# Kernel optimization log

Measured on AMD Instinct MI355X. Metric: run time of the kernel, lower is better.

## Reference

```python
import jax, jax.numpy as jnp
import numpy as np

N = 100000      # nodes (spots/cells)
IN = 512        # layers[0]: gene features
HID = 128       # layers[1]: GAT out_feats (num_heads=1)
OUT = 64        # layers[-1]: embedding dim
K = 20          # clusters
E_RAND = 800000 # random edges; + N self-loops => 900000 edges total
DEC_ALPHA = 1.0
NEG_SLOPE = 0.2  # DGL GATConv default leaky_relu slope


def setup_inputs() -> dict:
    key = jax.random.key(0)
    ks = jax.random.split(key, 9)
    x = jax.random.normal(ks[0], (N, IN), dtype=jnp.float32)
    # random edges + self-loops so every node has in-degree >= 1
    src = jnp.concatenate([jax.random.randint(ks[1], (E_RAND,), 0, N), jnp.arange(N)])
    dst = jnp.concatenate([jax.random.randint(ks[2], (E_RAND,), 0, N), jnp.arange(N)])
    W_gat = jax.random.normal(ks[3], (IN, HID), dtype=jnp.float32) * (1.0 / np.sqrt(IN))
    attn_l = jax.random.normal(ks[4], (HID,), dtype=jnp.float32) * 0.1
    attn_r = jax.random.normal(ks[5], (HID,), dtype=jnp.float32) * 0.1
    bias_gat = jnp.zeros((HID,), dtype=jnp.float32)
    # nn.Linear weights stored as (in, out) so forward is x @ W (same math as x @ W_torch.T)
    W_enc = jax.random.normal(ks[6], (HID, OUT), dtype=jnp.float32) * (1.0 / np.sqrt(HID))
    W_dec = jax.random.normal(ks[7], (OUT, IN), dtype=jnp.float32) * (1.0 / np.sqrt(OUT))
    centroids = jax.random.normal(ks[8], (K, OUT), dtype=jnp.float32)
    return {"x": x, "W_gat": W_gat, "attn_l": attn_l, "attn_r": attn_r,
            "bias_gat": bias_gat, "W_enc": W_enc, "W_dec": W_dec,
            "centroids": centroids, "src": src, "dst": dst}


def reference(x, W_gat, attn_l, attn_r, bias_gat, W_enc, W_dec, centroids, src, dst):
    # --- GATConv (single head, DGL semantics) ---
    h = x @ W_gat                                  # (N, HID)
    el = h @ attn_l                                # (N,)
    er = h @ attn_r                                # (N,)
    e = jax.nn.leaky_relu(el[src] + er[dst], NEG_SLOPE)          # (E,)
    m = jax.ops.segment_max(e, dst, num_segments=N)              # per-dst max for stable softmax
    a = jnp.exp(e - m[dst])
    denom = jax.ops.segment_sum(a, dst, num_segments=N)
    alpha = a / denom[dst]                                       # edge softmax over in-edges
    agg = jax.ops.segment_sum(alpha[:, None] * h[src], dst, num_segments=N) + bias_gat  # (N, HID)
    # --- encode ---
    embed = jax.nn.elu(agg) @ W_enc                # (N, OUT)
    # --- decode ---
    pred_gene = jax.nn.elu(embed @ W_dec)          # (N, IN)
    # --- DEC soft cluster assignment (Student-t kernel) ---
    d2 = (jnp.sum(embed * embed, axis=1, keepdims=True)
          + jnp.sum(centroids * centroids, axis=1)[None, :]
          - 2.0 * (embed @ centroids.T))           # (N, K) squared distances
    q = 1.0 / (1.0 + d2 / DEC_ALPHA + 1e-8)
    q = q ** ((DEC_ALPHA + 1.0) / 2.0)
    q = q / jnp.sum(q, axis=1, keepdims=True)
    return embed, pred_gene, q
```

## Files before the change

### kernel.cpp

```cpp
#include <hip/hip_runtime.h>
#include <math.h>

constexpr int IN   = 512;
constexpr int HID  = 128;
constexpr int OUTD = 64;
constexpr int KC   = 20;
#define LRELU_SLOPE 0.2f

typedef _Float16 half8 __attribute__((ext_vector_type(8)));
typedef _Float16 half2v __attribute__((ext_vector_type(2)));
typedef float f32x16 __attribute__((ext_vector_type(16)));

__device__ __forceinline__ float warp_sum(float v) {
#pragma unroll
  for (int o = 32; o > 0; o >>= 1) v += __shfl_xor(v, o, 64);
  return v;
}
__device__ __forceinline__ float group_sum16(float v) {
#pragma unroll
  for (int o = 8; o > 0; o >>= 1) v += __shfl_xor(v, o, 64);
  return v;
}

__global__ __launch_bounds__(256) void k_prep(const float* __restrict__ Wg,
                                              const float* __restrict__ We,
                                              const float* __restrict__ Wd,
                                              _Float16* Bg, _Float16* Be, _Float16* Bd,
                                              int* counts, int N) {
  int i = blockIdx.x * 256 + threadIdx.x;
  if (i < N) counts[i] = 0;
  if (i < HID * IN) {
    int c = i >> 9, k = i & 511;
    Bg[i] = (_Float16)Wg[(size_t)k * HID + c];
    return;
  }
  i -= HID * IN;
  if (i < OUTD * HID) {
    int c = i >> 7, k = i & 127;
    Be[i] = (_Float16)We[(size_t)k * OUTD + c];
    return;
  }
  i -= OUTD * HID;
  if (i < IN * OUTD) {
    int c = i >> 6, k = i & 63;
    Bd[i] = (_Float16)Wd[(size_t)k * IN + c];
  }
}

__global__ __launch_bounds__(256) void k_gemm1e(const float* __restrict__ A,
                                                const _Float16* __restrict__ Bt,
                                                const float* __restrict__ al,
                                                const float* __restrict__ ar,
                                                _Float16* __restrict__ H,
                                                float* __restrict__ el,
                                                float* __restrict__ er, int M) {
  __shared__ char smem[36864];
  _Float16* As = (_Float16*)smem;
  _Float16* Bs = (_Float16*)(smem + 18432);
  _Float16* Hs = (_Float16*)smem;
  float*    als = (float*)(smem + 34816);
  float*    ars = (float*)(smem + 35328);
  const int tid = threadIdx.x;
  const int lane = tid & 63, wid = tid >> 6;
  const int wrow = (wid >> 1) * 64, wcol = (wid & 1) * 64;
  const int row0 = blockIdx.x * 128;
  const int l31 = lane & 31, lhi = lane >> 5;

  f32x16 acc[2][2] = {};

  for (int k0 = 0; k0 < IN; k0 += 64) {
#pragma unroll
    for (int c = 0; c < 4; ++c) {
      int idx = tid + c * 256;
      int r = idx >> 3, ko = idx & 7;
      int gr = row0 + r;
      float4 v0 = make_float4(0.f, 0.f, 0.f, 0.f), v1 = v0;
      if (gr < M) {
        const float* p = A + (size_t)gr * IN + k0 + ko * 8;
        v0 = *(const float4*)p;
        v1 = *(const float4*)(p + 4);
      }
      half8 hv;
      hv[0] = (_Float16)v0.x; hv[1] = (_Float16)v0.y; hv[2] = (_Float16)v0.z; hv[3] = (_Float16)v0.w;
      hv[4] = (_Float16)v1.x; hv[5] = (_Float16)v1.y; hv[6] = (_Float16)v1.z; hv[7] = (_Float16)v1.w;
      *(half8*)(&As[r * 72 + ko * 8]) = hv;
    }
#pragma unroll
    for (int c = 0; c < 4; ++c) {
      int idx = tid + c * 256;
      int col = idx >> 3, ko = idx & 7;
      *(half8*)(&Bs[col * 72 + ko * 8]) = *(const half8*)(Bt + (size_t)col * IN + k0 + ko * 8);
    }
    __syncthreads();
#pragma unroll
    for (int ks = 0; ks < 4; ++ks) {
      half8 a0 = *(half8*)(&As[(wrow + l31) * 72      + ks * 16 + lhi * 8]);
      half8 a1 = *(half8*)(&As[(wrow + 32 + l31) * 72 + ks * 16 + lhi * 8]);
      half8 b0 = *(half8*)(&Bs[(wcol + l31) * 72      + ks * 16 + lhi * 8]);
      half8 b1 = *(half8*)(&Bs[(wcol + 32 + l31) * 72 + ks * 16 + lhi * 8]);
      acc[0][0] = __builtin_amdgcn_mfma_f32_32x32x16_f16(a0, b0, acc[0][0], 0, 0, 0);
      acc[0][1] = __builtin_amdgcn_mfma_f32_32x32x16_f16(a0, b1, acc[0][1], 0, 0, 0);
      acc[1][0] = __builtin_amdgcn_mfma_f32_32x32x16_f16(a1, b0, acc[1][0], 0, 0, 0);
      acc[1][1] = __builtin_amdgcn_mfma_f32_32x32x16_f16(a1, b1, acc[1][1], 0, 0, 0);
    }
    __syncthreads();
  }
  if (tid < 128) als[tid] = al[tid];
  else ars[tid - 128] = ar[tid - 128];
#pragma unroll
  for (int mr = 0; mr < 2; ++mr)
#pragma unroll
    for (int r = 0; r < 16; ++r) {
      int lr = wrow + mr * 32 + (r & 3) + 8 * (r >> 2) + 4 * lhi;
      int row = row0 + lr;
#pragma unroll
      for (int nr = 0; nr < 2; ++nr) {
        _Float16 hv = (_Float16)acc[mr][nr][r];
        Hs[lr * 136 + wcol + nr * 32 + l31] = hv;
        if (row < M) H[(size_t)row * HID + wcol + nr * 32 + l31] = hv;
      }
    }
  __syncthreads();
  if (tid < 128) {
    int row = row0 + tid;
    if (row < M) {
      float sl = 0.f, sr = 0.f;
#pragma unroll
      for (int c8 = 0; c8 < 16; ++c8) {
        half8 hv = *(half8*)(&Hs[tid * 136 + c8 * 8]);
#pragma unroll
        for (int j = 0; j < 8; ++j) {
          float hf = (float)hv[j];
          sl = fmaf(hf, als[c8 * 8 + j], sl);
          sr = fmaf(hf, ars[c8 * 8 + j], sr);
        }
      }
      el[row] = sl;
      er[row] = sr;
    }
  }
}

__global__ void k_hist(const int* __restrict__ dst, int* counts, int E) {
  int i = (blockIdx.x * blockDim.x + threadIdx.x) * 4;
  if (i + 4 <= E) {
    int4 d = *(const int4*)(dst + i);
    atomicAdd(&counts[d.x], 1); atomicAdd(&counts[d.y], 1);
    atomicAdd(&counts[d.z], 1); atomicAdd(&counts[d.w], 1);
  } else {
    for (; i < E; ++i) atomicAdd(&counts[dst[i]], 1);
  }
}

__global__ __launch_bounds__(256) void k_scan1(const int* __restrict__ counts, int* bsum, int N) {
  __shared__ int s[256];
  int b = blockIdx.x, t = threadIdx.x;
  int i0 = b * 512 + t * 2;
  int v = 0;
  if (i0 < N) v += counts[i0];
  if (i0 + 1 < N) v += counts[i0 + 1];
  s[t] = v;
  __syncthreads();
  for (int off = 128; off > 0; off >>= 1) {
    if (t < off) s[t] += s[t + off];
    __syncthreads();
  }
  if (t == 0) bsum[b] = s[0];
}

__global__ __launch_bounds__(256) void k_scan3m(const int* __restrict__ counts,
                                                const int* __restrict__ bsum,
                                                int* rowptr, int* cursor, int N, int nblk) {
  __shared__ int sb[256];
  __shared__ int s[256];
  int b = blockIdx.x, t = threadIdx.x;
  int v = (t < nblk) ? bsum[t] : 0;
  sb[t] = v;
  __syncthreads();
#pragma unroll
  for (int off = 1; off < 256; off <<= 1) {
    int u = 0;
    if (t >= off) u = sb[t - off];
    __syncthreads();
    sb[t] += u;
    __syncthreads();
  }
  int boffb = (b == 0) ? 0 : sb[b - 1];

  int i0 = b * 512 + t * 2;
  int c0 = (i0 < N) ? counts[i0] : 0;
  int c1 = (i0 + 1 < N) ? counts[i0 + 1] : 0;
  int tsum = c0 + c1;
  s[t] = tsum;
  __syncthreads();
#pragma unroll
  for (int off = 1; off < 256; off <<= 1) {
    int u = 0;
    if (t >= off) u = s[t - off];
    __syncthreads();
    s[t] += u;
    __syncthreads();
  }
  int base = boffb + s[t] - tsum;
  if (i0 < N)     { rowptr[i0] = base;          cursor[i0] = base; }
  if (i0 + 1 < N) { rowptr[i0 + 1] = base + c0; cursor[i0 + 1] = base + c0; }
}

__global__ void k_fill(const int* __restrict__ src, const int* __restrict__ dst,
                       const float* __restrict__ el, const float* __restrict__ er,
                       int* cursor, int2* colsw, int E) {
  int i = (blockIdx.x * blockDim.x + threadIdx.x) * 4;
  if (i + 4 <= E) {
    int4 sv = *(const int4*)(src + i);
    int4 dv = *(const int4*)(dst + i);
    float e0 = el[sv.x] + er[dv.x]; e0 = (e0 > 0.f) ? e0 : LRELU_SLOPE * e0;
    float e1 = el[sv.y] + er[dv.y]; e1 = (e1 > 0.f) ? e1 : LRELU_SLOPE * e1;
    float e2 = el[sv.z] + er[dv.z]; e2 = (e2 > 0.f) ? e2 : LRELU_SLOPE * e2;
    float e3 = el[sv.w] + er[dv.w]; e3 = (e3 > 0.f) ? e3 : LRELU_SLOPE * e3;
    float w0 = __expf(e0), w1 = __expf(e1), w2 = __expf(e2), w3 = __expf(e3);
    colsw[atomicAdd(&cursor[dv.x], 1)] = make_int2(sv.x, __float_as_int(w0));
    colsw[atomicAdd(&cursor[dv.y], 1)] = make_int2(sv.y, __float_as_int(w1));
    colsw[atomicAdd(&cursor[dv.z], 1)] = make_int2(sv.z, __float_as_int(w2));
    colsw[atomicAdd(&cursor[dv.w], 1)] = make_int2(sv.w, __float_as_int(w3));
  } else {
    for (; i < E; ++i) {
      int s = src[i], d = dst[i];
      float e = el[s] + er[d]; e = (e > 0.f) ? e : LRELU_SLOPE * e;
      colsw[atomicAdd(&cursor[d], 1)] = make_int2(s, __float_as_int(__expf(e)));
    }
  }
}

__global__ __launch_bounds__(256) void k_agg(const _Float16* __restrict__ h,
                                             const int* __restrict__ rowptr,
                                             const int* __restrict__ counts,
                                             const int2* __restrict__ colsw,
                                             const float* __restrict__ bias,
                                             _Float16* __restrict__ eh, int N) {
  int tid = threadIdx.x;
  int v = blockIdx.x * 16 + (tid >> 4);
  if (v >= N) return;
  int lane = tid & 63;
  int gidx = lane & 15;
  int grpb = lane & 48;
  int start = rowptr[v], deg = counts[v];

  float acc[8];
#pragma unroll
  for (int t = 0; t < 8; ++t) acc[t] = 0.f;
  float den = 0.f;

  for (int base = 0; base < deg; base += 16) {
    int cnt = deg - base; if (cnt > 16) cnt = 16;
    int u_l = 0; float w_l = 0.f;
    if (gidx < cnt) {
      int2 p = colsw[start + base + gidx];
      u_l = p.x;
      w_l = __int_as_float(p.y);
    }
    den += group_sum16(w_l);
    for (int j = 0; j < cnt; j += 4) {
      int   u0 = __shfl(u_l, grpb | (j + 0), 64), u1 = __shfl(u_l, grpb | (j + 1), 64);
      int   u2 = __shfl(u_l, grpb | (j + 2), 64), u3 = __shfl(u_l, grpb | (j + 3), 64);
      float w0 = __shfl(w_l, grpb | (j + 0), 64), w1 = __shfl(w_l, grpb | (j + 1), 64);
      float w2 = __shfl(w_l, grpb | (j + 2), 64), w3 = __shfl(w_l, grpb | (j + 3), 64);
      half8 h0 = *(const half8*)(h + (size_t)u0 * HID + gidx * 8);
      half8 h1 = *(const half8*)(h + (size_t)u1 * HID + gidx * 8);
      half8 h2 = *(const half8*)(h + (size_t)u2 * HID + gidx * 8);
      half8 h3 = *(const half8*)(h + (size_t)u3 * HID + gidx * 8);
#pragma unroll
      for (int t = 0; t < 8; ++t) {
        acc[t] = fmaf(w0, (float)h0[t], acc[t]);
        acc[t] = fmaf(w1, (float)h1[t], acc[t]);
        acc[t] = fmaf(w2, (float)h2[t], acc[t]);
        acc[t] = fmaf(w3, (float)h3[t], acc[t]);
      }
    }
  }
  float inv = 1.f / den;
  float4 b0 = *(const float4*)(bias + gidx * 8);
  float4 b1 = *(const float4*)(bias + gidx * 8 + 4);
  float bf[8] = {b0.x, b0.y, b0.z, b0.w, b1.x, b1.y, b1.z, b1.w};
  half8 o;
#pragma unroll
  for (int t = 0; t < 8; ++t) {
    float x = acc[t] * inv + bf[t];
    o[t] = (_Float16)((x > 0.f) ? x : (__expf(x) - 1.f));
  }
  *(half8*)(eh + (size_t)v * HID + gidx * 8) = o;
}

__global__ __launch_bounds__(256) void k_gemm2q(const _Float16* __restrict__ A,
                                                const _Float16* __restrict__ Bt,
                                                const float* __restrict__ cent,
                                                float* __restrict__ C,
                                                _Float16* __restrict__ C16,
                                                float* __restrict__ q, int M) {
  __shared__ _Float16 As[128 * 136];
  __shared__ _Float16 Bs[64 * 136];
  const int tid = threadIdx.x;
  const int lane = tid & 63, wid = tid >> 6;
  const int wrow = (wid >> 1) * 64, wcol = (wid & 1) * 32;
  const int row0 = blockIdx.x * 128;
  const int l31 = lane & 31, lhi = lane >> 5;

#pragma unroll
  for (int c = 0; c < 8; ++c) {
    int idx = tid + c * 256;
    int r = idx >> 4, ko = idx & 15;
    int gr = row0 + r;
    half8 hv = {};
    if (gr < M) hv = *(const half8*)(A + (size_t)gr * HID + ko * 8);
    *(half8*)(&As[r * 136 + ko * 8]) = hv;
  }
#pragma unroll
  for (int c = 0; c < 4; ++c) {
    int idx = tid + c * 256;
    int col = idx >> 4, ko = idx & 15;
    *(half8*)(&Bs[col * 136 + ko * 8]) = *(const half8*)(Bt + (size_t)col * HID + ko * 8);
  }
  __syncthreads();

  f32x16 acc[2] = {};
#pragma unroll
  for (int ks = 0; ks < 8; ++ks) {
    half8 a0 = *(half8*)(&As[(wrow + l31) * 136      + ks * 16 + lhi * 8]);
    half8 a1 = *(half8*)(&As[(wrow + 32 + l31) * 136 + ks * 16 + lhi * 8]);
    half8 b0 = *(half8*)(&Bs[(wcol + l31) * 136      + ks * 16 + lhi * 8]);
    acc[0] = __builtin_amdgcn_mfma_f32_32x32x16_f16(a0, b0, acc[0], 0, 0, 0);
    acc[1] = __builtin_amdgcn_mfma_f32_32x32x16_f16(a1, b0, acc[1], 0, 0, 0);
  }
  __syncthreads();

  float* Es = (float*)As;
  float* Cs = (float*)Bs;
#pragma unroll
  for (int t = 0; t < 5; ++t) {
    int i = tid + t * 256;
    if (i < KC * OUTD) Cs[i] = cent[i];
  }
#pragma unroll
  for (int mr = 0; mr < 2; ++mr)
#pragma unroll
    for (int r = 0; r < 16; ++r) {
      int lr = wrow + mr * 32 + (r & 3) + 8 * (r >> 2) + 4 * lhi;
      int row = row0 + lr;
      int col = wcol + l31;
      float x = acc[mr][r];
      Es[lr * 68 + col] = x;
      if (row < M) {
        C[(size_t)row * OUTD + col] = x;
        C16[(size_t)row * OUTD + col] = (_Float16)x;
      }
    }
  __syncthreads();

  if (tid < 128) {
    int row = row0 + tid;
    if (row < M) {
      const float* erow = &Es[tid * 68];
      float accq[KC];
#pragma unroll
      for (int k = 0; k < KC; ++k) accq[k] = 0.f;
#pragma unroll
      for (int d0 = 0; d0 < OUTD; d0 += 4) {
        float4 e4 = *(const float4*)(erow + d0);
#pragma unroll
        for (int k = 0; k < KC; ++k) {
          float4 c4 = *(const float4*)(&Cs[k * OUTD + d0]);
          float dx = e4.x - c4.x, dy = e4.y - c4.y, dz = e4.z - c4.z, dw = e4.w - c4.w;
          accq[k] = fmaf(dx, dx, fmaf(dy, dy, fmaf(dz, dz, fmaf(dw, dw, accq[k]))));
        }
      }
      float qs = 0.f;
#pragma unroll
      for (int k = 0; k < KC; ++k) {
        accq[k] = 1.f / (1.f + accq[k] + 1e-8f);
        qs += accq[k];
      }
      float inv = 1.f / qs;
      float* qrow = q + (size_t)row * KC;
#pragma unroll
      for (int k0 = 0; k0 < KC; k0 += 4) {
        float4 o = make_float4(accq[k0] * inv, accq[k0 + 1] * inv,
                               accq[k0 + 2] * inv, accq[k0 + 3] * inv);
        *(float4*)(qrow + k0) = o;
      }
    }
  }
}

__global__ __launch_bounds__(256) void k_gemm3(const _Float16* __restrict__ A,
                                               const _Float16* __restrict__ Bt,
                                               float* __restrict__ C, int M) {
  __shared__ _Float16 As[128 * 72];
  __shared__ _Float16 Bs[128 * 72];
  const int tid = threadIdx.x;
  const int lane = tid & 63, wid = tid >> 6;
  const int wrow = (wid >> 1) * 64, wcol = (wid & 1) * 64;
  const int row0 = blockIdx.x * 128;
  const int cb = blockIdx.y * 128;
  const int l31 = lane & 31, lhi = lane >> 5;

#pragma unroll
  for (int c = 0; c < 4; ++c) {
    int idx = tid + c * 256;
    int r = idx >> 3, ko = idx & 7;
    int gr = row0 + r;
    half8 hv = {};
    if (gr < M) hv = *(const half8*)(A + (size_t)gr * OUTD + ko * 8);
    *(half8*)(&As[r * 72 + ko * 8]) = hv;
  }
#pragma unroll
  for (int c = 0; c < 4; ++c) {
    int idx = tid + c * 256;
    int col = idx >> 3, ko = idx & 7;
    *(half8*)(&Bs[col * 72 + ko * 8]) = *(const half8*)(Bt + (size_t)(cb + col) * OUTD + ko * 8);
  }
  __syncthreads();

  f32x16 acc[2][2] = {};
#pragma unroll
  for (int ks = 0; ks < 4; ++ks) {
    half8 a0 = *(half8*)(&As[(wrow + l31) * 72      + ks * 16 + lhi * 8]);
    half8 a1 = *(half8*)(&As[(wrow + 32 + l31) * 72 + ks * 16 + lhi * 8]);
    half8 b0 = *(half8*)(&Bs[(wcol + l31) * 72      + ks * 16 + lhi * 8]);
    half8 b1 = *(half8*)(&Bs[(wcol + 32 + l31) * 72 + ks * 16 + lhi * 8]);
    acc[0][0] = __builtin_amdgcn_mfma_f32_32x32x16_f16(a0, b0, acc[0][0], 0, 0, 0);
    acc[0][1] = __builtin_amdgcn_mfma_f32_32x32x16_f16(a0, b1, acc[0][1], 0, 0, 0);
    acc[1][0] = __builtin_amdgcn_mfma_f32_32x32x16_f16(a1, b0, acc[1][0], 0, 0, 0);
    acc[1][1] = __builtin_amdgcn_mfma_f32_32x32x16_f16(a1, b1, acc[1][1], 0, 0, 0);
  }
#pragma unroll
  for (int mr = 0; mr < 2; ++mr)
#pragma unroll
    for (int r = 0; r < 16; ++r) {
      int row = row0 + wrow + mr * 32 + (r & 3) + 8 * (r >> 2) + 4 * lhi;
      if (row < M) {
#pragma unroll
        for (int nr = 0; nr < 2; ++nr) {
          float x = acc[mr][nr][r];
          C[(size_t)row * IN + cb + wcol + nr * 32 + l31] =
              (x > 0.f) ? x : (__expf(x) - 1.f);
        }
      }
    }
}

static inline size_t align16(size_t x) { return (x + 15) & ~(size_t)15; }

extern "C" void kernel_launch(void* const* d_in, const int* in_sizes, int n_in,
                              void* d_out, int out_size, void* d_ws, size_t ws_size,
                              hipStream_t stream) {
  const float* x      = (const float*)d_in[0];
  const float* W_gat  = (const float*)d_in[1];
  const float* attn_l = (const float*)d_in[2];
  const float* attn_r = (const float*)d_in[3];
  const float* bias   = (const float*)d_in[4];
  const float* W_enc  = (const float*)d_in[5];
  const float* W_dec  = (const float*)d_in[6];
  const float* cent   = (const float*)d_in[7];
  const int*   src    = (const int*)d_in[8];
  const int*   dst    = (const int*)d_in[9];

  const int N = in_sizes[0] / IN;
  const int E = in_sizes[8];

  float* out   = (float*)d_out;
  float* embed = out;
  float* pred  = out + (size_t)N * OUTD;
  float* qout  = pred + (size_t)N * IN;

  char* w = (char*)d_ws;
  size_t off = 0;
  _Float16* h16   = (_Float16*)(w + off); off = align16(off + sizeof(_Float16) * (size_t)N * HID);
  _Float16* eh16  = (_Float16*)(w + off); off = align16(off + sizeof(_Float16) * (size_t)N * HID);
  _Float16* emb16 = (_Float16*)(w + off); off = align16(off + sizeof(_Float16) * (size_t)N * OUTD);
  float* el       = (float*)(w + off);    off = align16(off + sizeof(float) * (size_t)N);
  float* er       = (float*)(w + off);    off = align16(off + sizeof(float) * (size_t)N);
  _Float16* Bt_g  = (_Float16*)(w + off); off = align16(off + sizeof(_Float16) * HID * IN);
  _Float16* Bt_e  = (_Float16*)(w + off); off = align16(off + sizeof(_Float16) * OUTD * HID);
  _Float16* Bt_d  = (_Float16*)(w + off); off = align16(off + sizeof(_Float16) * IN * OUTD);
  int* counts     = (int*)(w + off);      off = align16(off + sizeof(int) * (size_t)N);
  int* rowptr     = (int*)(w + off);      off = align16(off + sizeof(int) * (size_t)(N + 1));
  int* cursor     = (int*)(w + off);      off = align16(off + sizeof(int) * (size_t)N);
  int2* colsw     = (int2*)(w + off);     off = align16(off + sizeof(int2) * (size_t)E);
  int* bsum       = (int*)(w + off);      off = align16(off + sizeof(int) * 256);

  const int nblk_scan = (N + 511) / 512;
  const int prep_elems = HID * IN + OUTD * HID + IN * OUTD;
  const int nblk_prep = (prep_elems > N ? prep_elems : N);

  hipLaunchKernelGGL(k_prep, dim3((nblk_prep + 255) / 256), dim3(256), 0, stream,
                     W_gat, W_enc, W_dec, Bt_g, Bt_e, Bt_d, counts, N);
  hipLaunchKernelGGL(k_gemm1e, dim3((N + 127) / 128), dim3(256), 0, stream,
                     x, Bt_g, attn_l, attn_r, h16, el, er, N);
  hipLaunchKernelGGL(k_hist, dim3((E / 4 + 255) / 256), dim3(256), 0, stream, dst, counts, E);
  hipLaunchKernelGGL(k_scan1, dim3(nblk_scan), dim3(256), 0, stream, counts, bsum, N);
  hipLaunchKernelGGL(k_scan3m, dim3(nblk_scan), dim3(256), 0, stream,
                     counts, bsum, rowptr, cursor, N, nblk_scan);
  hipLaunchKernelGGL(k_fill, dim3((E / 4 + 255) / 256), dim3(256), 0, stream,
                     src, dst, el, er, cursor, colsw, E);
  hipLaunchKernelGGL(k_agg, dim3((N + 15) / 16), dim3(256), 0, stream,
                     h16, rowptr, counts, colsw, bias, eh16, N);
  hipLaunchKernelGGL(k_gemm2q, dim3((N + 127) / 128), dim3(256), 0, stream,
                     eh16, Bt_e, cent, embed, emb16, qout, N);
  hipLaunchKernelGGL(k_gemm3, dim3((N + 127) / 128, 4), dim3(256), 0, stream, emb16, Bt_d, pred, N);
}
```

Measured before the change: 291.3 us.

## Double-buffer GAT projection GEMM with register prefetch of next K tile

Rewrites the first GEMM main loop to prefetch the next 64-wide K slice of A and B into registers while MFMAs consume the current LDS buffer, then store it into the alternate LDS buffer. This halves the barriers per iteration and aims to hide global load latency behind compute. It doubles LDS use to about 73KB and adds launch_bounds(256,2), which raises register pressure and limits occupancy to two blocks per CU.

```diff
diff --git a/kernel.cpp b/kernel.cpp
--- a/kernel.cpp
+++ b/kernel.cpp
@@ -47,64 +47,91 @@
   }
 }
 
-__global__ __launch_bounds__(256) void k_gemm1e(const float* __restrict__ A,
-                                                const _Float16* __restrict__ Bt,
-                                                const float* __restrict__ al,
-                                                const float* __restrict__ ar,
-                                                _Float16* __restrict__ H,
-                                                float* __restrict__ el,
-                                                float* __restrict__ er, int M) {
-  __shared__ char smem[36864];
-  _Float16* As = (_Float16*)smem;
-  _Float16* Bs = (_Float16*)(smem + 18432);
-  _Float16* Hs = (_Float16*)smem;
-  float*    als = (float*)(smem + 34816);
-  float*    ars = (float*)(smem + 35328);
+__global__ __launch_bounds__(256, 2) void k_gemm1e(const float* __restrict__ A,
+                                                   const _Float16* __restrict__ Bt,
+                                                   const float* __restrict__ al,
+                                                   const float* __restrict__ ar,
+                                                   _Float16* __restrict__ H,
+                                                   float* __restrict__ el,
+                                                   float* __restrict__ er, int M) {
+  __shared__ char smem[74752];
+  _Float16* Hs  = (_Float16*)smem;
+  float*    als = (float*)(smem + 73728);
+  float*    ars = (float*)(smem + 74240);
   const int tid = threadIdx.x;
   const int lane = tid & 63, wid = tid >> 6;
   const int wrow = (wid >> 1) * 64, wcol = (wid & 1) * 64;
   const int row0 = blockIdx.x * 128;
   const int l31 = lane & 31, lhi = lane >> 5;
 
+  const int sr  = tid >> 3;
+  (void)sr;
+
   f32x16 acc[2][2] = {};
-
-  for (int k0 = 0; k0 < IN; k0 += 64) {
-#pragma unroll
-    for (int c = 0; c < 4; ++c) {
-      int idx = tid + c * 256;
-      int r = idx >> 3, ko = idx & 7;
-      int gr = row0 + r;
-      float4 v0 = make_float4(0.f, 0.f, 0.f, 0.f), v1 = v0;
-      if (gr < M) {
-        const float* p = A + (size_t)gr * IN + k0 + ko * 8;
-        v0 = *(const float4*)p;
-        v1 = *(const float4*)(p + 4);
-      }
-      half8 hv;
-      hv[0] = (_Float16)v0.x; hv[1] = (_Float16)v0.y; hv[2] = (_Float16)v0.z; hv[3] = (_Float16)v0.w;
-      hv[4] = (_Float16)v1.x; hv[5] = (_Float16)v1.y; hv[6] = (_Float16)v1.z; hv[7] = (_Float16)v1.w;
-      *(half8*)(&As[r * 72 + ko * 8]) = hv;
-    }
-#pragma unroll
-    for (int c = 0; c < 4; ++c) {
-      int idx = tid + c * 256;
-      int col = idx >> 3, ko = idx & 7;
-      *(half8*)(&Bs[col * 72 + ko * 8]) = *(const half8*)(Bt + (size_t)col * IN + k0 + ko * 8);
-    }
+  float4 a0r[4], a1r[4];
+  half8  br[4];
+
+#define G1_LOAD(K0)                                                        \
+  {                                                                        \
+    _Pragma("unroll")                                                      \
+    for (int c = 0; c < 4; ++c) {                                          \
+      int idx = tid + c * 256;                                             \
+      int r = idx >> 3, ko = idx & 7;                                      \
+      int gr = row0 + r;                                                   \
+      a0r[c] = make_float4(0.f, 0.f, 0.f, 0.f); a1r[c] = a0r[c];           \
+      if (gr < M) {                                                        \
+        const float* p = A + (size_t)gr * IN + (K0) + ko * 8;              \
+        a0r[c] = *(const float4*)p;                                        \
+        a1r[c] = *(const float4*)(p + 4);                                  \
+      }                                                                    \
+      br[c] = *(const half8*)(Bt + (size_t)r * IN + (K0) + ko * 8);        \
+    }                                                                      \
+  }
+
+#define G1_STORE(BUF)                                                      \
+  {                                                                        \
+    _Float16* Asb = (_Float16*)(smem + (BUF) * 36864);                     \
+    _Float16* Bsb = (_Float16*)(smem + (BUF) * 36864 + 18432);             \
+    _Pragma("unroll")                                                      \
+    for (int c = 0; c < 4; ++c) {                                          \
+      int idx = tid + c * 256;                                             \
+      int r = idx >> 3, ko = idx & 7;                                      \
+      half8 hv;                                                            \
+      hv[0] = (_Float16)a0r[c].x; hv[1] = (_Float16)a0r[c].y;              \
+      hv[2] = (_Float16)a0r[c].z; hv[3] = (_Float16)a0r[c].w;              \
+      hv[4] = (_Float16)a1r[c].x; hv[5] = (_Float16)a1r[c].y;              \
+      hv[6] = (_Float16)a1r[c].z; hv[7] = (_Float16)a1r[c].w;              \
+      *(half8*)(&Asb[r * 72 + ko * 8]) = hv;                               \
+      *(half8*)(&Bsb[r * 72 + ko * 8]) = br[c];                            \
+    }                                                                      \
+  }
+
+  G1_LOAD(0);
+  G1_STORE(0);
+
+#pragma unroll
+  for (int t = 0; t < 8; ++t) {
     __syncthreads();
-#pragma unroll
-    for (int ks = 0; ks < 4; ++ks) {
-      half8 a0 = *(half8*)(&As[(wrow + l31) * 72      + ks * 16 + lhi * 8]);
-      half8 a1 = *(half8*)(&As[(wrow + 32 + l31) * 72 + ks * 16 + lhi * 8]);
-      half8 b0 = *(half8*)(&Bs[(wcol + l31) * 72      + ks * 16 + lhi * 8]);
-      half8 b1 = *(half8*)(&Bs[(wcol + 32 + l31) * 72 + ks * 16 + lhi * 8]);
-      acc[0][0] = __builtin_amdgcn_mfma_f32_32x32x16_f16(a0, b0, acc[0][0], 0, 0, 0);
-      acc[0][1] = __builtin_amdgcn_mfma_f32_32x32x16_f16(a0, b1, acc[0][1], 0, 0, 0);
-      acc[1][0] = __builtin_amdgcn_mfma_f32_32x32x16_f16(a1, b0, acc[1][0], 0, 0, 0);
-      acc[1][1] = __builtin_amdgcn_mfma_f32_32x32x16_f16(a1, b1, acc[1][1], 0, 0, 0);
-    }
-    __syncthreads();
-  }
+    if (t < 7) G1_LOAD((t + 1) * 64);
+    {
+      const _Float16* Asb = (const _Float16*)(smem + (t & 1) * 36864);
+      const _Float16* Bsb = (const _Float16*)(smem + (t & 1) * 36864 + 18432);
+#pragma unroll
+      for (int ks = 0; ks < 4; ++ks) {
+        half8 a0 = *(const half8*)(&Asb[(wrow + l31) * 72      + ks * 16 + lhi * 8]);
+        half8 a1 = *(const half8*)(&Asb[(wrow + 32 + l31) * 72 + ks * 16 + lhi * 8]);
+        half8 b0 = *(const half8*)(&Bsb[(wcol + l31) * 72      + ks * 16 + lhi * 8]);
+        half8 b1 = *(const half8*)(&Bsb[(wcol + 32 + l31) * 72 + ks * 16 + lhi * 8]);
+        acc[0][0] = __builtin_amdgcn_mfma_f32_32x32x16_f16(a0, b0, acc[0][0], 0, 0, 0);
+        acc[0][1] = __builtin_amdgcn_mfma_f32_32x32x16_f16(a0, b1, acc[0][1], 0, 0, 0);
+        acc[1][0] = __builtin_amdgcn_mfma_f32_32x32x16_f16(a1, b0, acc[1][0], 0, 0, 0);
+        acc[1][1] = __builtin_amdgcn_mfma_f32_32x32x16_f16(a1, b1, acc[1][1], 0, 0, 0);
+      }
+    }
+    if (t < 7) G1_STORE((t + 1) & 1);
+  }
+  __syncthreads();
+
   if (tid < 128) als[tid] = al[tid];
   else ars[tid - 128] = ar[tid - 128];
 #pragma unroll
@@ -124,21 +151,23 @@
   if (tid < 128) {
     int row = row0 + tid;
     if (row < M) {
-      float sl = 0.f, sr = 0.f;
+      float sl = 0.f, sr2 = 0.f;
 #pragma unroll
       for (int c8 = 0; c8 < 16; ++c8) {
         half8 hv = *(half8*)(&Hs[tid * 136 + c8 * 8]);
 #pragma unroll
         for (int j = 0; j < 8; ++j) {
           float hf = (float)hv[j];
-          sl = fmaf(hf, als[c8 * 8 + j], sl);
-          sr = fmaf(hf, ars[c8 * 8 + j], sr);
+          sl  = fmaf(hf, als[c8 * 8 + j], sl);
+          sr2 = fmaf(hf, ars[c8 * 8 + j], sr2);
         }
       }
       el[row] = sl;
-      er[row] = sr;
-    }
-  }
+      er[row] = sr2;
+    }
+  }
+#undef G1_LOAD
+#undef G1_STORE
 }
 
 __global__ void k_hist(const int* __restrict__ dst, int* counts, int E) {
```

Result: slower. 298.1 us (+2.3%).
